# Optimization experiments

Hardware: AMD Instinct MI355X
Metric: run time of the kernel (lower is better)

The kernel has to match this reference:

```python
import jax, jax.numpy as jnp
import numpy as np

N = 100000   # nodes
E = 1600000  # edges
EL = 200000  # decode pairs
D_IN, D_HID, D_OUT = 128, 128, 64


def setup_inputs() -> dict:
    key = jax.random.key(0)
    ks = jax.random.split(key, 9)
    x = jax.random.normal(ks[0], (N, D_IN), dtype=jnp.float32)
    edge_index = jax.random.randint(ks[1], (2, E), 0, N, dtype=jnp.int64)
    edge_label_index = jax.random.randint(ks[2], (2, EL), 0, N, dtype=jnp.int64)
    # GCNConv params: weight [in, out] (no bias inside linear), bias added after aggregation
    W1 = jax.random.normal(ks[3], (D_IN, D_HID), dtype=jnp.float32) / np.sqrt(D_IN)
    b1 = jnp.zeros((D_HID,), dtype=jnp.float32)
    W2 = jax.random.normal(ks[4], (D_HID, D_HID), dtype=jnp.float32) / np.sqrt(D_HID)
    b2 = jnp.zeros((D_HID,), dtype=jnp.float32)
    W3 = jax.random.normal(ks[5], (D_HID, D_OUT), dtype=jnp.float32) / np.sqrt(D_HID)
    b3 = jnp.zeros((D_OUT,), dtype=jnp.float32)
    return {"x": x, "edge_index": edge_index, "edge_label_index": edge_label_index,
            "W1": W1, "b1": b1, "W2": W2, "b2": b2, "W3": W3, "b3": b3}


def _gcn_norm(edge_index, num_nodes, dtype):
    # add self-loops, compute symmetric normalization deg^-1/2[src]*deg^-1/2[dst]
    loop = jnp.arange(num_nodes, dtype=edge_index.dtype)
    src = jnp.concatenate([edge_index[0], loop])
    dst = jnp.concatenate([edge_index[1], loop])
    deg = jax.ops.segment_sum(jnp.ones(src.shape, dtype=dtype), dst, num_segments=num_nodes)
    dinv = jax.lax.rsqrt(deg)  # deg >= 1 due to self-loops
    norm = dinv[src] * dinv[dst]
    return src, dst, norm


def _gcn_conv(h, W, b, src, dst, norm, num_nodes):
    h = h @ W                               # [N, out]
    msg = h[src] * norm[:, None]            # gather + scale  [E+N, out]
    out = jax.ops.segment_sum(msg, dst, num_segments=num_nodes)  # scatter-add
    return out + b


def reference(x, edge_index, edge_label_index, W1, b1, W2, b2, W3, b3):
    num_nodes = x.shape[0]
    src, dst, norm = _gcn_norm(edge_index, num_nodes, x.dtype)
    h = jax.nn.relu(_gcn_conv(x, W1, b1, src, dst, norm, num_nodes))
    h = jax.nn.relu(_gcn_conv(h, W2, b2, src, dst, norm, num_nodes))  # dropout is identity in eval
    z = _gcn_conv(h, W3, b3, src, dst, norm, num_nodes)
    # decode: dot product over candidate pairs
    return jnp.sum(z[edge_label_index[0]] * z[edge_label_index[1]], axis=-1)
```

## Files before the change

kernel.cpp:

```cpp
#include <hip/hip_runtime.h>
#include <hip/hip_bf16.h>

#define N_NODES 100000
#define N_EDGES 1600000
#define N_EL    200000

#define NB_SCAN ((N_NODES + 255) / 256)
#define CPAD 16

typedef unsigned int uint32;
typedef unsigned short ushort16;
typedef __attribute__((ext_vector_type(8))) short short8;
typedef __attribute__((ext_vector_type(4))) float f32x4;

static __device__ __forceinline__ ushort16 f2bf(float f) {
    uint32 u = __float_as_uint(f);
    u += 0x7fffu + ((u >> 16) & 1u);
    return (ushort16)(u >> 16);
}
static __device__ __forceinline__ float bf_lo(uint32 p) { return __uint_as_float(p << 16); }
static __device__ __forceinline__ float bf_hi(uint32 p) { return __uint_as_float(p & 0xffff0000u); }
static __device__ __forceinline__ float bf2f(ushort16 h) { return __uint_as_float((uint32)h << 16); }

__global__ void k_rank(const int* __restrict__ dst, int* __restrict__ cpad,
                       int* __restrict__ r) {
    int e = blockIdx.x * blockDim.x + threadIdx.x;
    if (e < N_EDGES) r[e] = atomicAdd(&cpad[(size_t)dst[e] * CPAD], 1);
}

__global__ void k_scan1(const int* __restrict__ cpad, int* __restrict__ rowptr,
                        int* __restrict__ bsum, float* __restrict__ dinv) {
    __shared__ int s[256];
    int t = threadIdx.x;
    int i = blockIdx.x * 256 + t;
    int v = (i < N_NODES) ? cpad[(size_t)i * CPAD] : 0;
    if (i < N_NODES) dinv[i] = 1.0f / sqrtf((float)(v + 1));
    s[t] = v;
    __syncthreads();
    for (int off = 1; off < 256; off <<= 1) {
        int u = (t >= off) ? s[t - off] : 0;
        __syncthreads();
        s[t] += u;
        __syncthreads();
    }
    if (i < N_NODES) rowptr[i] = s[t] - v;
    if (t == 255) bsum[blockIdx.x] = s[255];
}

__global__ void k_scan2(const int* __restrict__ bsum, int* __restrict__ boff) {
    __shared__ int s[512];
    int t = threadIdx.x;
    int v = (t < NB_SCAN) ? bsum[t] : 0;
    s[t] = v;
    __syncthreads();
    for (int off = 1; off < 512; off <<= 1) {
        int u = (t >= off) ? s[t - off] : 0;
        __syncthreads();
        s[t] += u;
        __syncthreads();
    }
    if (t < NB_SCAN) boff[t] = s[t] - v;
    if (t == NB_SCAN - 1) boff[NB_SCAN] = s[t];
}

__global__ void k_scan3(int* __restrict__ rowptr, const int* __restrict__ boff) {
    int i = blockIdx.x * 256 + threadIdx.x;
    if (i < N_NODES) rowptr[i] += boff[blockIdx.x];
    if (i == 0) rowptr[N_NODES] = boff[NB_SCAN];
}

__global__ void k_fill2(const int* __restrict__ src, const int* __restrict__ dst,
                        const int* __restrict__ rowptr, const int* __restrict__ r,
                        int* __restrict__ col) {
    int e = blockIdx.x * blockDim.x + threadIdx.x;
    if (e >= N_EDGES) return;
    int pos = rowptr[dst[e]] + r[e];
    __builtin_nontemporal_store(src[e], &col[pos]);
}

static __device__ __forceinline__ short8 load_afrag(const float* arow, int off) {
    float4 a0 = *(const float4*)(arow + off);
    float4 a1 = *(const float4*)(arow + off + 4);
    short8 af;
    af[0] = (short)f2bf(a0.x); af[1] = (short)f2bf(a0.y);
    af[2] = (short)f2bf(a0.z); af[3] = (short)f2bf(a0.w);
    af[4] = (short)f2bf(a1.x); af[5] = (short)f2bf(a1.y);
    af[6] = (short)f2bf(a1.z); af[7] = (short)f2bf(a1.w);
    return af;
}
static __device__ __forceinline__ short8 load_afrag(const ushort16* arow, int off) {
    return *(const short8*)(arow + off);
}

template <int D, typename AT>
__global__ __launch_bounds__(256, 4) void k_gemm_mfma(const AT* __restrict__ A,
        const float* __restrict__ W, const float* __restrict__ dinv,
        ushort16* __restrict__ C) {
    constexpr int NT = D / 16;
    __shared__ short sB[4 * NT * 64 * 8];

    int tid = threadIdx.x;

    for (int idx = tid; idx < 128 * D; idx += 256) {
        int k = idx / D;
        int n = idx % D;
        int kt = k >> 5, kr = k & 31;
        int q = kr >> 3, j = kr & 7;
        int nt = n >> 4, nn = n & 15;
        sB[(((kt * NT + nt) * 64) + q * 16 + nn) * 8 + j] = (short)f2bf(W[idx]);
    }
    __syncthreads();

    int w = tid >> 6;
    int l = tid & 63;
    int q = l >> 4;
    int nn15 = l & 15;
    int m0 = blockIdx.x * 64 + w * 16;

    f32x4 acc[NT];
#pragma unroll
    for (int i = 0; i < NT; ++i) acc[i] = (f32x4){0.f, 0.f, 0.f, 0.f};

    int m = m0 + nn15;
    m = min(m, N_NODES - 1);
    const AT* arow = A + (size_t)m * 128;

#pragma unroll
    for (int kt = 0; kt < 4; ++kt) {
        short8 af = load_afrag(arow, kt * 32 + q * 8);
#pragma unroll
        for (int nt = 0; nt < NT; ++nt) {
            short8 bf = *(const short8*)&sB[((kt * NT + nt) * 64 + l) * 8];
            acc[nt] = __builtin_amdgcn_mfma_f32_16x16x32_bf16(af, bf, acc[nt], 0, 0, 0);
        }
    }

    float4 dv = *(const float4*)(dinv + m0 + 4 * q);
    const float* dvp = (const float*)&dv;
#pragma unroll
    for (int nt = 0; nt < NT; ++nt) {
#pragma unroll
        for (int r = 0; r < 4; ++r) {
            int node = m0 + q * 4 + r;
            if (node < N_NODES) {
                float val = acc[nt][r] * dvp[r];
                C[(size_t)node * D + nt * 16 + nn15] = f2bf(val);
            }
        }
    }
}

template <bool RELU>
__global__ void k_gather128(const int* __restrict__ rowptr, const int* __restrict__ col,
                            const float* __restrict__ dinv, const uint32* __restrict__ t,
                            const float* __restrict__ b, uint32* __restrict__ outbuf) {
    unsigned wid = (blockIdx.x * blockDim.x + threadIdx.x) >> 6;
    int lane = threadIdx.x & 63;
    if (wid >= N_NODES) return;
    int beg = rowptr[wid], end = rowptr[wid + 1];
    uint32 p = t[(size_t)wid * 64 + lane];
    float ax = bf_lo(p), ay = bf_hi(p);
    int j = beg;
    for (; j + 8 <= end; j += 8) {
        int s0 = col[j], s1 = col[j+1], s2 = col[j+2], s3 = col[j+3];
        int s4 = col[j+4], s5 = col[j+5], s6 = col[j+6], s7 = col[j+7];
        uint32 v0 = t[(size_t)s0 * 64 + lane];
        uint32 v1 = t[(size_t)s1 * 64 + lane];
        uint32 v2 = t[(size_t)s2 * 64 + lane];
        uint32 v3 = t[(size_t)s3 * 64 + lane];
        uint32 v4 = t[(size_t)s4 * 64 + lane];
        uint32 v5 = t[(size_t)s5 * 64 + lane];
        uint32 v6 = t[(size_t)s6 * 64 + lane];
        uint32 v7 = t[(size_t)s7 * 64 + lane];
        ax += (bf_lo(v0) + bf_lo(v1)) + (bf_lo(v2) + bf_lo(v3))
            + ((bf_lo(v4) + bf_lo(v5)) + (bf_lo(v6) + bf_lo(v7)));
        ay += (bf_hi(v0) + bf_hi(v1)) + (bf_hi(v2) + bf_hi(v3))
            + ((bf_hi(v4) + bf_hi(v5)) + (bf_hi(v6) + bf_hi(v7)));
    }
    for (; j + 4 <= end; j += 4) {
        int s0 = col[j], s1 = col[j+1], s2 = col[j+2], s3 = col[j+3];
        uint32 v0 = t[(size_t)s0 * 64 + lane];
        uint32 v1 = t[(size_t)s1 * 64 + lane];
        uint32 v2 = t[(size_t)s2 * 64 + lane];
        uint32 v3 = t[(size_t)s3 * 64 + lane];
        ax += (bf_lo(v0) + bf_lo(v1)) + (bf_lo(v2) + bf_lo(v3));
        ay += (bf_hi(v0) + bf_hi(v1)) + (bf_hi(v2) + bf_hi(v3));
    }
    for (; j < end; ++j) {
        uint32 v = t[(size_t)col[j] * 64 + lane];
        ax += bf_lo(v); ay += bf_hi(v);
    }
    float di = dinv[wid];
    float2 bb = ((const float2*)b)[lane];
    float ox = di * ax + bb.x;
    float oy = di * ay + bb.y;
    if (RELU) { ox = fmaxf(ox, 0.f); oy = fmaxf(oy, 0.f); }
    outbuf[(size_t)wid * 64 + lane] = (uint32)f2bf(ox) | ((uint32)f2bf(oy) << 16);
}

template <bool RELU>
__global__ void k_gather64(const int* __restrict__ rowptr, const int* __restrict__ col,
                           const float* __restrict__ dinv, const ushort16* __restrict__ t,
                           const float* __restrict__ b, ushort16* __restrict__ outbuf) {
    unsigned wid = (blockIdx.x * blockDim.x + threadIdx.x) >> 6;
    int lane = threadIdx.x & 63;
    if (wid >= N_NODES) return;
    int beg = rowptr[wid], end = rowptr[wid + 1];
    float acc = bf2f(t[(size_t)wid * 64 + lane]);
    int j = beg;
    for (; j + 8 <= end; j += 8) {
        int s0 = col[j], s1 = col[j+1], s2 = col[j+2], s3 = col[j+3];
        int s4 = col[j+4], s5 = col[j+5], s6 = col[j+6], s7 = col[j+7];
        float v0 = bf2f(t[(size_t)s0 * 64 + lane]);
        float v1 = bf2f(t[(size_t)s1 * 64 + lane]);
        float v2 = bf2f(t[(size_t)s2 * 64 + lane]);
        float v3 = bf2f(t[(size_t)s3 * 64 + lane]);
        float v4 = bf2f(t[(size_t)s4 * 64 + lane]);
        float v5 = bf2f(t[(size_t)s5 * 64 + lane]);
        float v6 = bf2f(t[(size_t)s6 * 64 + lane]);
        float v7 = bf2f(t[(size_t)s7 * 64 + lane]);
        acc += (v0 + v1) + (v2 + v3) + ((v4 + v5) + (v6 + v7));
    }
    for (; j + 4 <= end; j += 4) {
        int s0 = col[j], s1 = col[j+1], s2 = col[j+2], s3 = col[j+3];
        acc += (bf2f(t[(size_t)s0 * 64 + lane]) + bf2f(t[(size_t)s1 * 64 + lane]))
             + (bf2f(t[(size_t)s2 * 64 + lane]) + bf2f(t[(size_t)s3 * 64 + lane]));
    }
    for (; j < end; ++j) acc += bf2f(t[(size_t)col[j] * 64 + lane]);
    float o = dinv[wid] * acc + b[lane];
    if (RELU) o = fmaxf(o, 0.f);
    outbuf[(size_t)wid * 64 + lane] = f2bf(o);
}

__global__ void k_decode(const int* __restrict__ eli, const ushort16* __restrict__ z,
                         float* __restrict__ out) {
    int e = blockIdx.x * blockDim.x + threadIdx.x;
    if (e >= N_EL) return;
    int a = eli[e];
    int b = eli[N_EL + e];
    const uint4* za = (const uint4*)(z + (size_t)a * 64);
    const uint4* zb = (const uint4*)(z + (size_t)b * 64);
    float acc = 0.0f;
#pragma unroll
    for (int i = 0; i < 8; ++i) {
        uint4 va = za[i], vb = zb[i];
        acc += bf_lo(va.x) * bf_lo(vb.x) + bf_hi(va.x) * bf_hi(vb.x);
        acc += bf_lo(va.y) * bf_lo(vb.y) + bf_hi(va.y) * bf_hi(vb.y);
        acc += bf_lo(va.z) * bf_lo(vb.z) + bf_hi(va.z) * bf_hi(vb.z);
        acc += bf_lo(va.w) * bf_lo(vb.w) + bf_hi(va.w) * bf_hi(vb.w);
    }
    out[e] = acc;
}

extern "C" void kernel_launch(void* const* d_in, const int* in_sizes, int n_in,
                              void* d_out, int out_size, void* d_ws, size_t ws_size,
                              hipStream_t stream) {
    const float* x   = (const float*)d_in[0];
    const int*   ei  = (const int*)d_in[1];
    const int*   eli = (const int*)d_in[2];
    const float* W1  = (const float*)d_in[3];
    const float* b1  = (const float*)d_in[4];
    const float* W2  = (const float*)d_in[5];
    const float* b2  = (const float*)d_in[6];
    const float* W3  = (const float*)d_in[7];
    const float* b3  = (const float*)d_in[8];
    float* out = (float*)d_out;

    const int* srcA = ei;
    const int* dstA = ei + N_EDGES;

    char* ws = (char*)d_ws;
    float*    dinv   = (float*)   (ws + 0);
    int*      rowptr = (int*)     (ws + (1024u << 10));
    int*      bsum   = (int*)     (ws + (1888u << 10));
    int*      boff   = (int*)     (ws + (1896u << 10));
    int*      col    = (int*)     (ws + (2048u << 10));
    int*      r      = (int*)     (ws + (9u << 20));
    ushort16* t      = (ushort16*)(ws + (16u << 20));
    ushort16* aggb   = (ushort16*)(ws + (48u << 20));
    int*      cpad   = (int*)     (ws + (80u << 20));

    const int B = 256;
    const int gE  = (N_EDGES + B - 1) / B;
    const int gG  = (N_NODES * 64 + B - 1) / B;
    const int gT  = (N_NODES + 63) / 64;
    const int gEL = (N_EL + B - 1) / B;

    hipMemsetAsync(cpad, 0, (size_t)N_NODES * CPAD * sizeof(int), stream);
    k_rank<<<gE, B, 0, stream>>>(dstA, cpad, r);
    k_scan1<<<NB_SCAN, 256, 0, stream>>>(cpad, rowptr, bsum, dinv);
    k_scan2<<<1, 512, 0, stream>>>(bsum, boff);
    k_scan3<<<NB_SCAN, 256, 0, stream>>>(rowptr, boff);
    k_fill2<<<gE, B, 0, stream>>>(srcA, dstA, rowptr, r, col);

    k_gemm_mfma<128, float><<<gT, B, 0, stream>>>(x, W1, dinv, t);
    k_gather128<true><<<gG, B, 0, stream>>>(rowptr, col, dinv, (const uint32*)t, b1,
                                            (uint32*)aggb);
    k_gemm_mfma<128, ushort16><<<gT, B, 0, stream>>>(aggb, W2, dinv, t);
    k_gather128<true><<<gG, B, 0, stream>>>(rowptr, col, dinv, (const uint32*)t, b2,
                                            (uint32*)aggb);
    k_gemm_mfma<64, ushort16><<<gT, B, 0, stream>>>(aggb, W3, dinv, t);
    k_gather64<false><<<gG, B, 0, stream>>>(rowptr, col, dinv, t, b3, aggb);

    k_decode<<<gEL, B, 0, stream>>>(eli, aggb, out);
}
```

Measured before the change: 490.4 us.

## Fuse first GEMM with edge ranking and move source-degree scaling into gathers

The first-layer GEMM no longer depends on dinv, so it is merged into one launch with the edge-ranking atomics, with blocks split by index. The source-side dinv scaling moves out of the GEMM epilogue and into the gather kernels. Each wave now stages up to 64 neighbour indices and their dinv values in LDS and accumulates with FMAs. Output stores become nontemporal. This removes a launch and lets GEMM work overlap with the atomics, at the cost of an extra random dinv read per edge in every gather.

After: 449.3 us. 1.09x faster.

```diff
diff --git a/kernel.cpp b/kernel.cpp
--- a/kernel.cpp
+++ b/kernel.cpp
@@ -7,6 +7,7 @@
 
 #define NB_SCAN ((N_NODES + 255) / 256)
 #define CPAD 16
+#define GT_GEMM ((N_NODES + 63) / 64)
 
 typedef unsigned int uint32;
 typedef unsigned short ushort16;
@@ -21,12 +22,6 @@
 static __device__ __forceinline__ float bf_lo(uint32 p) { return __uint_as_float(p << 16); }
 static __device__ __forceinline__ float bf_hi(uint32 p) { return __uint_as_float(p & 0xffff0000u); }
 static __device__ __forceinline__ float bf2f(ushort16 h) { return __uint_as_float((uint32)h << 16); }
-
-__global__ void k_rank(const int* __restrict__ dst, int* __restrict__ cpad,
-                       int* __restrict__ r) {
-    int e = blockIdx.x * blockDim.x + threadIdx.x;
-    if (e < N_EDGES) r[e] = atomicAdd(&cpad[(size_t)dst[e] * CPAD], 1);
-}
 
 __global__ void k_scan1(const int* __restrict__ cpad, int* __restrict__ rowptr,
                         int* __restrict__ bsum, float* __restrict__ dinv) {
@@ -93,9 +88,8 @@
 }
 
 template <int D, typename AT>
-__global__ __launch_bounds__(256, 4) void k_gemm_mfma(const AT* __restrict__ A,
-        const float* __restrict__ W, const float* __restrict__ dinv,
-        ushort16* __restrict__ C) {
+static __device__ __forceinline__ void gemm_body(int bid, const AT* __restrict__ A,
+        const float* __restrict__ W, ushort16* __restrict__ C) {
     constexpr int NT = D / 16;
     __shared__ short sB[4 * NT * 64 * 8];
 
@@ -115,7 +109,7 @@
     int l = tid & 63;
     int q = l >> 4;
     int nn15 = l & 15;
-    int m0 = blockIdx.x * 64 + w * 16;
+    int m0 = bid * 64 + w * 16;
 
     f32x4 acc[NT];
 #pragma unroll
@@ -135,18 +129,31 @@
         }
     }
 
-    float4 dv = *(const float4*)(dinv + m0 + 4 * q);
-    const float* dvp = (const float*)&dv;
 #pragma unroll
     for (int nt = 0; nt < NT; ++nt) {
 #pragma unroll
         for (int r = 0; r < 4; ++r) {
             int node = m0 + q * 4 + r;
-            if (node < N_NODES) {
-                float val = acc[nt][r] * dvp[r];
-                C[(size_t)node * D + nt * 16 + nn15] = f2bf(val);
-            }
+            if (node < N_NODES)
+                C[(size_t)node * D + nt * 16 + nn15] = f2bf(acc[nt][r]);
         }
+    }
+}
+
+template <int D, typename AT>
+__global__ __launch_bounds__(256, 4) void k_gemm_mfma(const AT* __restrict__ A,
+        const float* __restrict__ W, ushort16* __restrict__ C) {
+    gemm_body<D, AT>(blockIdx.x, A, W, C);
+}
+
+__global__ __launch_bounds__(256, 4) void k_fat1(const float* __restrict__ A,
+        const float* __restrict__ W, ushort16* __restrict__ C,
+        const int* __restrict__ dst, int* __restrict__ cpad, int* __restrict__ r) {
+    if (blockIdx.x < GT_GEMM) {
+        gemm_body<128, float>(blockIdx.x, A, W, C);
+    } else {
+        int e = (blockIdx.x - GT_GEMM) * 256 + threadIdx.x;
+        if (e < N_EDGES) r[e] = atomicAdd(&cpad[(size_t)dst[e] * CPAD], 1);
     }
 }
 
@@ -154,82 +161,102 @@
 __global__ void k_gather128(const int* __restrict__ rowptr, const int* __restrict__ col,
                             const float* __restrict__ dinv, const uint32* __restrict__ t,
                             const float* __restrict__ b, uint32* __restrict__ outbuf) {
-    unsigned wid = (blockIdx.x * blockDim.x + threadIdx.x) >> 6;
-    int lane = threadIdx.x & 63;
+    __shared__ int   sc[4][64];
+    __shared__ float sd[4][64];
+    int tid = threadIdx.x;
+    unsigned wid = (blockIdx.x * 256u + tid) >> 6;
     if (wid >= N_NODES) return;
+    int w = tid >> 6;
+    int lane = tid & 63;
     int beg = rowptr[wid], end = rowptr[wid + 1];
+    float di = dinv[wid];
     uint32 p = t[(size_t)wid * 64 + lane];
-    float ax = bf_lo(p), ay = bf_hi(p);
-    int j = beg;
-    for (; j + 8 <= end; j += 8) {
-        int s0 = col[j], s1 = col[j+1], s2 = col[j+2], s3 = col[j+3];
-        int s4 = col[j+4], s5 = col[j+5], s6 = col[j+6], s7 = col[j+7];
-        uint32 v0 = t[(size_t)s0 * 64 + lane];
-        uint32 v1 = t[(size_t)s1 * 64 + lane];
-        uint32 v2 = t[(size_t)s2 * 64 + lane];
-        uint32 v3 = t[(size_t)s3 * 64 + lane];
-        uint32 v4 = t[(size_t)s4 * 64 + lane];
-        uint32 v5 = t[(size_t)s5 * 64 + lane];
-        uint32 v6 = t[(size_t)s6 * 64 + lane];
-        uint32 v7 = t[(size_t)s7 * 64 + lane];
-        ax += (bf_lo(v0) + bf_lo(v1)) + (bf_lo(v2) + bf_lo(v3))
-            + ((bf_lo(v4) + bf_lo(v5)) + (bf_lo(v6) + bf_lo(v7)));
-        ay += (bf_hi(v0) + bf_hi(v1)) + (bf_hi(v2) + bf_hi(v3))
-            + ((bf_hi(v4) + bf_hi(v5)) + (bf_hi(v6) + bf_hi(v7)));
-    }
-    for (; j + 4 <= end; j += 4) {
-        int s0 = col[j], s1 = col[j+1], s2 = col[j+2], s3 = col[j+3];
-        uint32 v0 = t[(size_t)s0 * 64 + lane];
-        uint32 v1 = t[(size_t)s1 * 64 + lane];
-        uint32 v2 = t[(size_t)s2 * 64 + lane];
-        uint32 v3 = t[(size_t)s3 * 64 + lane];
-        ax += (bf_lo(v0) + bf_lo(v1)) + (bf_lo(v2) + bf_lo(v3));
-        ay += (bf_hi(v0) + bf_hi(v1)) + (bf_hi(v2) + bf_hi(v3));
-    }
-    for (; j < end; ++j) {
-        uint32 v = t[(size_t)col[j] * 64 + lane];
-        ax += bf_lo(v); ay += bf_hi(v);
-    }
-    float di = dinv[wid];
+    float ax = di * bf_lo(p), ay = di * bf_hi(p);
+    for (int base = beg; base < end; base += 64) {
+        int cnt = min(end - base, 64);
+        int c = 0;
+        if (lane < cnt) c = col[base + lane];
+        sc[w][lane] = c;
+        float cd = (lane < cnt) ? dinv[c] : 0.f;
+        sd[w][lane] = cd;
+        int nb = (cnt + 7) >> 3;
+        for (int j8 = 0; j8 < nb; ++j8) {
+            int j = j8 << 3;
+            int s0 = sc[w][j+0], s1 = sc[w][j+1], s2 = sc[w][j+2], s3 = sc[w][j+3];
+            int s4 = sc[w][j+4], s5 = sc[w][j+5], s6 = sc[w][j+6], s7 = sc[w][j+7];
+            uint32 v0 = t[(size_t)s0 * 64 + lane];
+            uint32 v1 = t[(size_t)s1 * 64 + lane];
+            uint32 v2 = t[(size_t)s2 * 64 + lane];
+            uint32 v3 = t[(size_t)s3 * 64 + lane];
+            uint32 v4 = t[(size_t)s4 * 64 + lane];
+            uint32 v5 = t[(size_t)s5 * 64 + lane];
+            uint32 v6 = t[(size_t)s6 * 64 + lane];
+            uint32 v7 = t[(size_t)s7 * 64 + lane];
+            float d0 = sd[w][j+0], d1 = sd[w][j+1], d2 = sd[w][j+2], d3 = sd[w][j+3];
+            float d4 = sd[w][j+4], d5 = sd[w][j+5], d6 = sd[w][j+6], d7 = sd[w][j+7];
+            ax = fmaf(d0, bf_lo(v0), ax); ay = fmaf(d0, bf_hi(v0), ay);
+            ax = fmaf(d1, bf_lo(v1), ax); ay = fmaf(d1, bf_hi(v1), ay);
+            ax = fmaf(d2, bf_lo(v2), ax); ay = fmaf(d2, bf_hi(v2), ay);
+            ax = fmaf(d3, bf_lo(v3), ax); ay = fmaf(d3, bf_hi(v3), ay);
+            ax = fmaf(d4, bf_lo(v4), ax); ay = fmaf(d4, bf_hi(v4), ay);
+            ax = fmaf(d5, bf_lo(v5), ax); ay = fmaf(d5, bf_hi(v5), ay);
+            ax = fmaf(d6, bf_lo(v6), ax); ay = fmaf(d6, bf_hi(v6), ay);
+            ax = fmaf(d7, bf_lo(v7), ax); ay = fmaf(d7, bf_hi(v7), ay);
+        }
+    }
     float2 bb = ((const float2*)b)[lane];
     float ox = di * ax + bb.x;
     float oy = di * ay + bb.y;
     if (RELU) { ox = fmaxf(ox, 0.f); oy = fmaxf(oy, 0.f); }
-    outbuf[(size_t)wid * 64 + lane] = (uint32)f2bf(ox) | ((uint32)f2bf(oy) << 16);
+    __builtin_nontemporal_store((uint32)f2bf(ox) | ((uint32)f2bf(oy) << 16),
+                                &outbuf[(size_t)wid * 64 + lane]);
 }
 
 template <bool RELU>
 __global__ void k_gather64(const int* __restrict__ rowptr, const int* __restrict__ col,
                            const float* __restrict__ dinv, const ushort16* __restrict__ t,
                            const float* __restrict__ b, ushort16* __restrict__ outbuf) {
-    unsigned wid = (blockIdx.x * blockDim.x + threadIdx.x) >> 6;
-    int lane = threadIdx.x & 63;
+    __shared__ int   sc[4][64];
+    __shared__ float sd[4][64];
+    int tid = threadIdx.x;
+    unsigned wid = (blockIdx.x * 256u + tid) >> 6;
     if (wid >= N_NODES) return;
+    int w = tid >> 6;
+    int lane = tid & 63;
     int beg = rowptr[wid], end = rowptr[wid + 1];
-    float acc = bf2f(t[(size_t)wid * 64 + lane]);
-    int j = beg;
-    for (; j + 8 <= end; j += 8) {
-        int s0 = col[j], s1 = col[j+1], s2 = col[j+2], s3 = col[j+3];
-        int s4 = col[j+4], s5 = col[j+5], s6 = col[j+6], s7 = col[j+7];
-        float v0 = bf2f(t[(size_t)s0 * 64 + lane]);
-        float v1 = bf2f(t[(size_t)s1 * 64 + lane]);
-        float v2 = bf2f(t[(size_t)s2 * 64 + lane]);
-        float v3 = bf2f(t[(size_t)s3 * 64 + lane]);
-        float v4 = bf2f(t[(size_t)s4 * 64 + lane]);
-        float v5 = bf2f(t[(size_t)s5 * 64 + lane]);
-        float v6 = bf2f(t[(size_t)s6 * 64 + lane]);
-        float v7 = bf2f(t[(size_t)s7 * 64 + lane]);
-        acc += (v0 + v1) + (v2 + v3) + ((v4 + v5) + (v6 + v7));
-    }
-    for (; j + 4 <= end; j += 4) {
-        int s0 = col[j], s1 = col[j+1], s2 = col[j+2], s3 = col[j+3];
-        acc += (bf2f(t[(size_t)s0 * 64 + lane]) + bf2f(t[(size_t)s1 * 64 + lane]))
-             + (bf2f(t[(size_t)s2 * 64 + lane]) + bf2f(t[(size_t)s3 * 64 + lane]));
-    }
-    for (; j < end; ++j) acc += bf2f(t[(size_t)col[j] * 64 + lane]);
-    float o = dinv[wid] * acc + b[lane];
+    float di = dinv[wid];
+    float acc = di * bf2f(t[(size_t)wid * 64 + lane]);
+    for (int base = beg; base < end; base += 64) {
+        int cnt = min(end - base, 64);
+        int c = 0;
+        if (lane < cnt) c = col[base + lane];
+        sc[w][lane] = c;
+        float cd = (lane < cnt) ? dinv[c] : 0.f;
+        sd[w][lane] = cd;
+        int nb = (cnt + 7) >> 3;
+        for (int j8 = 0; j8 < nb; ++j8) {
+            int j = j8 << 3;
+            int s0 = sc[w][j+0], s1 = sc[w][j+1], s2 = sc[w][j+2], s3 = sc[w][j+3];
+            int s4 = sc[w][j+4], s5 = sc[w][j+5], s6 = sc[w][j+6], s7 = sc[w][j+7];
+            float v0 = bf2f(t[(size_t)s0 * 64 + lane]);
+            float v1 = bf2f(t[(size_t)s1 * 64 + lane]);
+            float v2 = bf2f(t[(size_t)s2 * 64 + lane]);
+            float v3 = bf2f(t[(size_t)s3 * 64 + lane]);
+            float v4 = bf2f(t[(size_t)s4 * 64 + lane]);
+            float v5 = bf2f(t[(size_t)s5 * 64 + lane]);
+            float v6 = bf2f(t[(size_t)s6 * 64 + lane]);
+            float v7 = bf2f(t[(size_t)s7 * 64 + lane]);
+            float d0 = sd[w][j+0], d1 = sd[w][j+1], d2 = sd[w][j+2], d3 = sd[w][j+3];
+            float d4 = sd[w][j+4], d5 = sd[w][j+5], d6 = sd[w][j+6], d7 = sd[w][j+7];
+            acc = fmaf(d0, v0, acc); acc = fmaf(d1, v1, acc);
+            acc = fmaf(d2, v2, acc); acc = fmaf(d3, v3, acc);
+            acc = fmaf(d4, v4, acc); acc = fmaf(d5, v5, acc);
+            acc = fmaf(d6, v6, acc); acc = fmaf(d7, v7, acc);
+        }
+    }
+    float o = di * acc + b[lane];
     if (RELU) o = fmaxf(o, 0.f);
-    outbuf[(size_t)wid * 64 + lane] = f2bf(o);
+    __builtin_nontemporal_store(f2bf(o), &outbuf[(size_t)wid * 64 + lane]);
 }
 
 __global__ void k_decode(const int* __restrict__ eli, const ushort16* __restrict__ z,
@@ -283,23 +310,21 @@
     const int B = 256;
     const int gE  = (N_EDGES + B - 1) / B;
     const int gG  = (N_NODES * 64 + B - 1) / B;
-    const int gT  = (N_NODES + 63) / 64;
     const int gEL = (N_EL + B - 1) / B;
 
     hipMemsetAsync(cpad, 0, (size_t)N_NODES * CPAD * sizeof(int), stream);
-    k_rank<<<gE, B, 0, stream>>>(dstA, cpad, r);
+    k_fat1<<<GT_GEMM + gE, B, 0, stream>>>(x, W1, t, dstA, cpad, r);
     k_scan1<<<NB_SCAN, 256, 0, stream>>>(cpad, rowptr, bsum, dinv);
     k_scan2<<<1, 512, 0, stream>>>(bsum, boff);
     k_scan3<<<NB_SCAN, 256, 0, stream>>>(rowptr, boff);
     k_fill2<<<gE, B, 0, stream>>>(srcA, dstA, rowptr, r, col);
 
-    k_gemm_mfma<128, float><<<gT, B, 0, stream>>>(x, W1, dinv, t);
     k_gather128<true><<<gG, B, 0, stream>>>(rowptr, col, dinv, (const uint32*)t, b1,
                                             (uint32*)aggb);
-    k_gemm_mfma<128, ushort16><<<gT, B, 0, stream>>>(aggb, W2, dinv, t);
+    k_gemm_mfma<128, ushort16><<<GT_GEMM, B, 0, stream>>>(aggb, W2, t);
     k_gather128<true><<<gG, B, 0, stream>>>(rowptr, col, dinv, (const uint32*)t, b2,
                                             (uint32*)aggb);
-    k_gemm_mfma<64, ushort16><<<gT, B, 0, stream>>>(aggb, W3, dinv, t);
+    k_gemm_mfma<64, ushort16><<<GT_GEMM, B, 0, stream>>>(aggb, W3, t);
     k_gather64<false><<<gG, B, 0, stream>>>(rowptr, col, dinv, t, b3, aggb);
 
     k_decode<<<gEL, B, 0, stream>>>(eli, aggb, out);
```
